# Optimization experiments

Measured on AMD Instinct MI355X. Metric: run time of the kernel, lower is better.

## Reference

```python
import jax, jax.numpy as jnp
import numpy as np

B, N, C, H = 4, 2048, 1024, 16
D = C // H  # head dim


def setup_inputs() -> dict:
    key = jax.random.key(0)
    ks = jax.random.split(key, 9)
    s = 1.0 / np.sqrt(C)
    inp = {"x": jax.random.normal(ks[0], (B, N, C), dtype=jnp.float32)}
    names = ["wq", "wk", "wv", "wo"]
    for i, n in enumerate(names):
        inp[n] = jax.random.uniform(ks[1 + 2 * i], (C, C), dtype=jnp.float32, minval=-s, maxval=s)
        inp["b" + n[1]] = jax.random.uniform(ks[2 + 2 * i], (C,), dtype=jnp.float32, minval=-s, maxval=s)
    return inp


def reference(x, wq, bq, wk, bk, wv, bv, wo, bo):
    b, n, c = x.shape
    # projections; weights stored as (in, out) so y = x @ w + b
    def split_heads(y):
        return y.reshape(b, n, H, D).transpose(0, 2, 1, 3)  # (B,H,N,D)

    q = split_heads(x @ wq + bq)
    k = split_heads(x @ wk + bk)
    v = split_heads(x @ wv + bv)
    scores = jnp.einsum("bhnd,bhmd->bhnm", q, k) / np.sqrt(D).astype(x.dtype)
    attn = jax.nn.softmax(scores, axis=-1)
    ctx = jnp.einsum("bhnm,bhmd->bhnd", attn, v)
    out = ctx.transpose(0, 2, 1, 3).reshape(b, n, c)
    return out @ wo + bo
```

## Files before the change

### kernel.cpp

```cpp
#include <hip/hip_runtime.h>
#include <hip/hip_bf16.h>
#include <hip/hip_fp16.h>

#define SEQ 2048
#define NH  16
#define DH  64
#define CH  1024
#define BATCH 4
#define BH (BATCH*NH)
#define MTOK (BATCH*SEQ)

typedef unsigned short u16;
typedef _Float16 h8 __attribute__((ext_vector_type(8)));
typedef float f4 __attribute__((ext_vector_type(4)));
typedef float f16x __attribute__((ext_vector_type(16)));

#define AS1(p) ((const __attribute__((address_space(1))) unsigned int*)(p))
#define AS3(p) ((__attribute__((address_space(3))) unsigned int*)(p))

__device__ __forceinline__ u16 f2h(float f) {
  _Float16 h = (_Float16)f;
  return __builtin_bit_cast(unsigned short, h);
}

__device__ __forceinline__ unsigned cvtpk(float a, float b) {
  auto t = __builtin_amdgcn_cvt_pkrtz(a, b);
  return __builtin_bit_cast(unsigned, t);
}

__device__ __forceinline__ float ex2(float x) { return __builtin_amdgcn_exp2f(x); }

__global__ __launch_bounds__(256) void k_convert_x(const float* __restrict__ x,
                                                   u16* __restrict__ xh) {
  int idx = (blockIdx.x * 256 + threadIdx.x) * 8;
  float4 a = *(const float4*)(x + idx);
  float4 b = *(const float4*)(x + idx + 4);
  uint4 o;
  o.x = (unsigned)f2h(a.x) | ((unsigned)f2h(a.y) << 16);
  o.y = (unsigned)f2h(a.z) | ((unsigned)f2h(a.w) << 16);
  o.z = (unsigned)f2h(b.x) | ((unsigned)f2h(b.y) << 16);
  o.w = (unsigned)f2h(b.z) | ((unsigned)f2h(b.w) << 16);
  *(uint4*)(xh + idx) = o;
}

__global__ __launch_bounds__(256) void k_transpose_w(const float* __restrict__ w0,
                                                     const float* __restrict__ w1,
                                                     const float* __restrict__ w2,
                                                     const float* __restrict__ w3,
                                                     u16* __restrict__ dst_all) {
  int mat = blockIdx.z;
  const float* src = (mat == 0) ? w0 : (mat == 1) ? w1 : (mat == 2) ? w2 : w3;
  u16* dst = dst_all + (size_t)mat * (CH * CH);
  __shared__ float t[64][65];
  int n0 = blockIdx.x * 64, k0 = blockIdx.y * 64;
#pragma unroll
  for (int i = 0; i < 16; ++i) {
    int idx = threadIdx.x + i * 256;
    int r = idx >> 6, c = idx & 63;
    t[r][c] = src[(size_t)(k0 + r) * CH + n0 + c];
  }
  __syncthreads();
#pragma unroll
  for (int i = 0; i < 16; ++i) {
    int idx = threadIdx.x + i * 256;
    int r = idx >> 6, c = idx & 63;
    dst[(size_t)(n0 + r) * CH + k0 + c] = f2h(t[c][r]);
  }
}

__global__ __launch_bounds__(256) void k_transpose_v(const u16* __restrict__ v,
                                                     u16* __restrict__ vt) {
  int n0 = blockIdx.x * 64;
  int bh = blockIdx.y;
  __shared__ u16 t[64][68];
  const u16* src = v + (size_t)bh * SEQ * DH + (size_t)n0 * DH;
#pragma unroll
  for (int i = 0; i < 4; ++i) {
    int g = threadIdx.x + i * 256;
    int r = g >> 4, c4 = (g & 15) * 4;
    *(ushort4*)&t[r][c4] = *(const ushort4*)(src + (size_t)r * DH + c4);
  }
  __syncthreads();
  u16* dst = vt + (size_t)bh * DH * SEQ + n0;
#pragma unroll
  for (int i = 0; i < 4; ++i) {
    int g = threadIdx.x + i * 256;
    int d = g >> 4, k4 = (g & 15) * 4;
    ushort4 o;
    o.x = t[k4 + 0][d]; o.y = t[k4 + 1][d]; o.z = t[k4 + 2][d]; o.w = t[k4 + 3][d];
    *(ushort4*)(dst + (size_t)d * SEQ + k4) = o;
  }
}

__global__ __launch_bounds__(256) void k_gemm_qkv(
    const u16* __restrict__ xh, const u16* __restrict__ wt,
    const float* __restrict__ bq, const float* __restrict__ bk,
    const float* __restrict__ bv,
    u16* __restrict__ qo, u16* __restrict__ ko, u16* __restrict__ vo) {
  const int tid = threadIdx.x;
  const int lane = tid & 63;
  const int wv = tid >> 6;
  const int wr = wv >> 1, wc = wv & 1;
  const int l16 = lane & 15, g = lane >> 4;
  const int tm = blockIdx.x;
  const int tn = blockIdx.y;
  const int mat = tn >> 3;
  const int nbase = (tn & 7) * 128;
  const u16* wb = wt + (size_t)mat * (CH * CH);

  __shared__ u16 As[128 * 32];
  __shared__ u16 Bs[128 * 32];

  f4 zero = {0.f, 0.f, 0.f, 0.f};
  f4 acc[4][4];
#pragma unroll
  for (int m = 0; m < 4; ++m)
#pragma unroll
    for (int n = 0; n < 4; ++n) acc[m][n] = zero;

  for (int k0 = 0; k0 < CH; k0 += 32) {
#pragma unroll
    for (int j = 0; j < 2; ++j) {
      int rbase = wv * 32 + j * 16;
      int row = rbase + (lane >> 2);
      int blk = (lane & 3) ^ ((row >> 1) & 3);
      const u16* ga = xh + (size_t)(tm * 128 + row) * CH + k0 + blk * 8;
      __builtin_amdgcn_global_load_lds(AS1(ga), AS3(&As[rbase * 32]), 16, 0, 0);
      const u16* gb = wb + (size_t)(nbase + row) * CH + k0 + blk * 8;
      __builtin_amdgcn_global_load_lds(AS1(gb), AS3(&Bs[rbase * 32]), 16, 0, 0);
    }
    __syncthreads();

    h8 af[4], bf[4];
#pragma unroll
    for (int i = 0; i < 4; ++i) {
      int arow = wr * 64 + i * 16 + l16;
      af[i] = *(const h8*)&As[arow * 32 + ((g ^ ((arow >> 1) & 3)) * 8)];
      int brow = wc * 64 + i * 16 + l16;
      bf[i] = *(const h8*)&Bs[brow * 32 + ((g ^ ((brow >> 1) & 3)) * 8)];
    }
#pragma unroll
    for (int m = 0; m < 4; ++m)
#pragma unroll
      for (int n = 0; n < 4; ++n)
        acc[m][n] = __builtin_amdgcn_mfma_f32_16x16x32_f16(af[m], bf[n], acc[m][n], 0, 0, 0);
    __syncthreads();
  }

  const float* bias = (mat == 0) ? bq : (mat == 1) ? bk : bv;
  u16* outp = (mat == 0) ? qo : (mat == 1) ? ko : vo;
  const float qscale = (mat == 0) ? 0.125f * 1.44269504f : 1.0f;
#pragma unroll
  for (int n = 0; n < 4; ++n) {
    int col = nbase + wc * 64 + n * 16 + l16;
    float bcol = bias[col];
    int h_ = col >> 6, d_ = col & 63;
#pragma unroll
    for (int m = 0; m < 4; ++m) {
#pragma unroll
      for (int r = 0; r < 4; ++r) {
        int t = tm * 128 + wr * 64 + m * 16 + g * 4 + r;
        int b_ = t >> 11, nseq = t & 2047;
        float val = (acc[m][n][r] + bcol) * qscale;
        outp[(((size_t)(b_ * NH + h_) * SEQ) + nseq) * DH + d_] = f2h(val);
      }
    }
  }
}

__global__ __launch_bounds__(256, 4) void k_attn(const u16* __restrict__ q,
                                                 const u16* __restrict__ k,
                                                 const u16* __restrict__ vt,
                                                 u16* __restrict__ ctx) {
  const int bid = blockIdx.x;
  const int bh = ((bid & 7) << 3) | ((bid >> 3) & 7);
  const int qb0 = bid >> 6;
  const int tid = threadIdx.x;
  const int lane = tid & 63;
  const int w = tid >> 6;
  const int l31 = lane & 31;
  const int hi = lane >> 5;

  __shared__ u16 Ks[2][32 * 128];
  __shared__ u16 Vs[2][32 * 128];

  const u16* kbase = k + (size_t)bh * SEQ * DH;
  const u16* vbase = vt + (size_t)bh * DH * SEQ;
  const u16* qbase = q + (size_t)bh * SEQ * DH;
  const int q0 = qb0 * 128 + w * 32;

  h8 qf[4];
#pragma unroll
  for (int ds = 0; ds < 4; ++ds)
    qf[ds] = *(const h8*)(qbase + (size_t)(q0 + l31) * DH + 16 * ds + 8 * hi);

  int koff[2][4];
  int voff[2][2][2];
#pragma unroll
  for (int h = 0; h < 2; ++h) {
#pragma unroll
    for (int ds = 0; ds < 4; ++ds) {
      int slot = 8 * h + 2 * ds + hi;
      koff[h][ds] = l31 * 128 + ((slot ^ (l31 & 15)) * 8);
    }
#pragma unroll
    for (int db = 0; db < 2; ++db)
#pragma unroll
      for (int ks = 0; ks < 2; ++ks) {
        int slot = 8 * db + 4 * h + 2 * ks + hi;
        voff[h][db][ks] = l31 * 128 + ((slot ^ (l31 & 15)) * 8);
      }
  }

  const u16* gk[2];
  const u16* gv[2];
#pragma unroll
  for (int c = 0; c < 2; ++c) {
    int r2 = w * 8 + c * 4 + (lane >> 4);
    int S = (lane & 15) ^ (r2 & 15);
    gk[c] = kbase + (size_t)(r2 + 32 * (S >> 3)) * DH + (S & 7) * 8;
    gv[c] = vbase + (size_t)(r2 + 32 * (S >> 3)) * SEQ + (S & 7) * 8;
  }

  const f16x fzero = {};
  h8 vones;
  {
    unsigned o1 = 0x3C003C00u;
    uint4 t = {o1, o1, o1, o1};
    vones = __builtin_bit_cast(h8, t);
  }

  f16x accq[2];
  accq[0] = {}; accq[1] = {};
  f16x lsum = {};

  auto STAGE = [&](int bi) {
#pragma unroll
    for (int c = 0; c < 2; ++c) {
      __builtin_amdgcn_global_load_lds(AS1(gk[c]), AS3(&Ks[bi][(w * 8 + c * 4) * 128]), 16, 0, 0);
      __builtin_amdgcn_global_load_lds(AS1(gv[c]), AS3(&Vs[bi][(w * 8 + c * 4) * 128]), 16, 0, 0);
      gk[c] += 64 * DH;
      gv[c] += 64;
    }
  };

  auto pack8 = [&](const float* p, int ks) -> h8 {
    unsigned a0 = cvtpk(p[8 * ks + 0], p[8 * ks + 1]);
    unsigned c0 = cvtpk(p[8 * ks + 2], p[8 * ks + 3]);
    unsigned b0 = cvtpk(p[8 * ks + 4], p[8 * ks + 5]);
    unsigned d0 = cvtpk(p[8 * ks + 6], p[8 * ks + 7]);
    unsigned s1 = __shfl_xor(hi ? a0 : b0, 32, 64);
    unsigned s2 = __shfl_xor(hi ? c0 : d0, 32, 64);
    uint4 wds;
    wds.x = hi ? s1 : a0;
    wds.y = hi ? s2 : c0;
    wds.z = hi ? b0 : s1;
    wds.w = hi ? d0 : s2;
    return __builtin_bit_cast(h8, wds);
  };

  auto SUBSTEP = [&](const u16* Kb, const u16* Vb, int h) {
    h8 kf0 = *(const h8*)(Kb + koff[h][0]);
    __builtin_amdgcn_s_setprio(1);
    f16x s = __builtin_amdgcn_mfma_f32_32x32x16_f16(kf0, qf[0], fzero, 0, 0, 0);
#pragma unroll
    for (int ds = 1; ds < 4; ++ds) {
      h8 kf = *(const h8*)(Kb + koff[h][ds]);
      s = __builtin_amdgcn_mfma_f32_32x32x16_f16(kf, qf[ds], s, 0, 0, 0);
    }
    __builtin_amdgcn_s_setprio(0);
    float p[16];
#pragma unroll
    for (int r = 0; r < 16; ++r) p[r] = ex2(s[r]);

    h8 pa0 = pack8(p, 0);
    h8 pa1 = pack8(p, 1);
    __builtin_amdgcn_s_setprio(1);
    lsum = __builtin_amdgcn_mfma_f32_32x32x16_f16(pa0, vones, lsum, 0, 0, 0);
    lsum = __builtin_amdgcn_mfma_f32_32x32x16_f16(pa1, vones, lsum, 0, 0, 0);
#pragma unroll
    for (int db = 0; db < 2; ++db) {
      h8 vf0 = *(const h8*)(Vb + voff[h][db][0]);
      accq[db] = __builtin_amdgcn_mfma_f32_32x32x16_f16(pa0, vf0, accq[db], 0, 0, 0);
      h8 vf1 = *(const h8*)(Vb + voff[h][db][1]);
      accq[db] = __builtin_amdgcn_mfma_f32_32x32x16_f16(pa1, vf1, accq[db], 0, 0, 0);
    }
    __builtin_amdgcn_s_setprio(0);
  };

  STAGE(0);
  for (int kt = 0; kt < SEQ / 64; kt += 2) {
    __syncthreads();
    STAGE(1);
    SUBSTEP(&Ks[0][0], &Vs[0][0], 0);
    SUBSTEP(&Ks[0][0], &Vs[0][0], 1);
    __syncthreads();
    if (kt + 2 < SEQ / 64) STAGE(0);
    SUBSTEP(&Ks[1][0], &Vs[1][0], 0);
    SUBSTEP(&Ks[1][0], &Vs[1][0], 1);
  }

  int b_ = bh >> 4, h_ = bh & 15;
#pragma unroll
  for (int r = 0; r < 16; ++r) {
    int row = (r & 3) + 8 * (r >> 2) + 4 * hi;
    float i0 = 1.0f / lsum[r];
#pragma unroll
    for (int db = 0; db < 2; ++db) {
      ctx[((size_t)(b_ * SEQ + q0 + row)) * CH + h_ * 64 + 32 * db + l31] =
          f2h(accq[db][r] * i0);
    }
  }
}

__global__ __launch_bounds__(256) void k_gemm_out(const u16* __restrict__ ctxb,
                                                  const u16* __restrict__ wot,
                                                  const float* __restrict__ bo,
                                                  float* __restrict__ out) {
  const int tid = threadIdx.x;
  const int lane = tid & 63;
  const int wv = tid >> 6;
  const int wr = wv >> 1, wc = wv & 1;
  const int l16 = lane & 15, g = lane >> 4;
  const int tm = blockIdx.x;
  const int nbase = blockIdx.y * 128;

  __shared__ u16 As[128 * 32];
  __shared__ u16 Bs[128 * 32];

  f4 zero = {0.f, 0.f, 0.f, 0.f};
  f4 acc[4][4];
#pragma unroll
  for (int m = 0; m < 4; ++m)
#pragma unroll
    for (int n = 0; n < 4; ++n) acc[m][n] = zero;

  for (int k0 = 0; k0 < CH; k0 += 32) {
#pragma unroll
    for (int j = 0; j < 2; ++j) {
      int rbase = wv * 32 + j * 16;
      int row = rbase + (lane >> 2);
      int blk = (lane & 3) ^ ((row >> 1) & 3);
      const u16* ga = ctxb + (size_t)(tm * 128 + row) * CH + k0 + blk * 8;
      __builtin_amdgcn_global_load_lds(AS1(ga), AS3(&As[rbase * 32]), 16, 0, 0);
      const u16* gb = wot + (size_t)(nbase + row) * CH + k0 + blk * 8;
      __builtin_amdgcn_global_load_lds(AS1(gb), AS3(&Bs[rbase * 32]), 16, 0, 0);
    }
    __syncthreads();

    h8 af[4], bf[4];
#pragma unroll
    for (int i = 0; i < 4; ++i) {
      int arow = wr * 64 + i * 16 + l16;
      af[i] = *(const h8*)&As[arow * 32 + ((g ^ ((arow >> 1) & 3)) * 8)];
      int brow = wc * 64 + i * 16 + l16;
      bf[i] = *(const h8*)&Bs[brow * 32 + ((g ^ ((brow >> 1) & 3)) * 8)];
    }
#pragma unroll
    for (int m = 0; m < 4; ++m)
#pragma unroll
      for (int n = 0; n < 4; ++n)
        acc[m][n] = __builtin_amdgcn_mfma_f32_16x16x32_f16(af[m], bf[n], acc[m][n], 0, 0, 0);
    __syncthreads();
  }

#pragma unroll
  for (int n = 0; n < 4; ++n) {
    int col = nbase + wc * 64 + n * 16 + l16;
    float bcol = bo[col];
#pragma unroll
    for (int m = 0; m < 4; ++m) {
#pragma unroll
      for (int r = 0; r < 4; ++r) {
        int t = tm * 128 + wr * 64 + m * 16 + g * 4 + r;
        out[(size_t)t * CH + col] = acc[m][n][r] + bcol;
      }
    }
  }
}

extern "C" void kernel_launch(void* const* d_in, const int* in_sizes, int n_in,
                              void* d_out, int out_size, void* d_ws, size_t ws_size,
                              hipStream_t stream) {
  (void)in_sizes; (void)n_in; (void)out_size; (void)ws_size;
  const float* x  = (const float*)d_in[0];
  const float* wq = (const float*)d_in[1];
  const float* bq = (const float*)d_in[2];
  const float* wk = (const float*)d_in[3];
  const float* bk = (const float*)d_in[4];
  const float* wv = (const float*)d_in[5];
  const float* bv = (const float*)d_in[6];
  const float* wo = (const float*)d_in[7];
  const float* bo = (const float*)d_in[8];
  float* out = (float*)d_out;

  char* ws = (char*)d_ws;
  u16* xh   = (u16*)(ws);
  u16* wt   = (u16*)(ws + 16777216);
  u16* qbuf = (u16*)(ws + 25165824);
  u16* kbuf = (u16*)(ws + 41943040);
  u16* vbuf = (u16*)(ws + 58720256);
  u16* ctxb = (u16*)(ws + 75497472);
  u16* wot  = wt + 3 * CH * CH;
  u16* vtb  = xh;

  k_convert_x<<<dim3(4096), dim3(256), 0, stream>>>(x, xh);
  k_transpose_w<<<dim3(16, 16, 4), dim3(256), 0, stream>>>(wq, wk, wv, wo, wt);
  k_gemm_qkv<<<dim3(64, 24), dim3(256), 0, stream>>>(xh, wt, bq, bk, bv, qbuf, kbuf, vbuf);
  k_transpose_v<<<dim3(32, 64), dim3(256), 0, stream>>>(vbuf, vtb);
  k_attn<<<dim3(1024), dim3(256), 0, stream>>>(qbuf, kbuf, vtb, ctxb);
  k_gemm_out<<<dim3(64, 8), dim3(256), 0, stream>>>(ctxb, wot, bo, out);
}
```

Measured before the change: 200.0 us.

## Double-buffer LDS in projection GEMMs and write V transposed directly

Both projection GEMMs now use two LDS buffers so the global-to-LDS load of the next K slice overlaps the MFMA work on the current one, and the per-iteration index math is hoisted into pointers that are simply advanced. The QKV GEMM epilogue writes V straight into the (B·H, D, N) transposed layout with 4-wide stores, so the separate V transpose kernel and its extra read and write pass are removed. The cost is doubled LDS per block, which may lower occupancy, and V stores that are strided across d.

```diff
diff --git a/kernel.cpp b/kernel.cpp
--- a/kernel.cpp
+++ b/kernel.cpp
@@ -68,35 +68,11 @@
   }
 }
 
-__global__ __launch_bounds__(256) void k_transpose_v(const u16* __restrict__ v,
-                                                     u16* __restrict__ vt) {
-  int n0 = blockIdx.x * 64;
-  int bh = blockIdx.y;
-  __shared__ u16 t[64][68];
-  const u16* src = v + (size_t)bh * SEQ * DH + (size_t)n0 * DH;
-#pragma unroll
-  for (int i = 0; i < 4; ++i) {
-    int g = threadIdx.x + i * 256;
-    int r = g >> 4, c4 = (g & 15) * 4;
-    *(ushort4*)&t[r][c4] = *(const ushort4*)(src + (size_t)r * DH + c4);
-  }
-  __syncthreads();
-  u16* dst = vt + (size_t)bh * DH * SEQ + n0;
-#pragma unroll
-  for (int i = 0; i < 4; ++i) {
-    int g = threadIdx.x + i * 256;
-    int d = g >> 4, k4 = (g & 15) * 4;
-    ushort4 o;
-    o.x = t[k4 + 0][d]; o.y = t[k4 + 1][d]; o.z = t[k4 + 2][d]; o.w = t[k4 + 3][d];
-    *(ushort4*)(dst + (size_t)d * SEQ + k4) = o;
-  }
-}
-
 __global__ __launch_bounds__(256) void k_gemm_qkv(
     const u16* __restrict__ xh, const u16* __restrict__ wt,
     const float* __restrict__ bq, const float* __restrict__ bk,
     const float* __restrict__ bv,
-    u16* __restrict__ qo, u16* __restrict__ ko, u16* __restrict__ vo) {
+    u16* __restrict__ qo, u16* __restrict__ ko, u16* __restrict__ vo_t) {
   const int tid = threadIdx.x;
   const int lane = tid & 63;
   const int wv = tid >> 6;
@@ -108,8 +84,21 @@
   const int nbase = (tn & 7) * 128;
   const u16* wb = wt + (size_t)mat * (CH * CH);
 
-  __shared__ u16 As[128 * 32];
-  __shared__ u16 Bs[128 * 32];
+  __shared__ u16 As[2][128 * 32];
+  __shared__ u16 Bs[2][128 * 32];
+
+  const u16* gA[2];
+  const u16* gB[2];
+  int rbase_[2];
+#pragma unroll
+  for (int j = 0; j < 2; ++j) {
+    int rbase = wv * 32 + j * 16;
+    rbase_[j] = rbase;
+    int row = rbase + (lane >> 2);
+    int blk = (lane & 3) ^ ((row >> 1) & 3);
+    gA[j] = xh + (size_t)(tm * 128 + row) * CH + blk * 8;
+    gB[j] = wb + (size_t)(nbase + row) * CH + blk * 8;
+  }
 
   f4 zero = {0.f, 0.f, 0.f, 0.f};
   f4 acc[4][4];
@@ -118,51 +107,78 @@
 #pragma unroll
     for (int n = 0; n < 4; ++n) acc[m][n] = zero;
 
-  for (int k0 = 0; k0 < CH; k0 += 32) {
+  auto STAGE = [&](int bi) {
 #pragma unroll
     for (int j = 0; j < 2; ++j) {
-      int rbase = wv * 32 + j * 16;
-      int row = rbase + (lane >> 2);
-      int blk = (lane & 3) ^ ((row >> 1) & 3);
-      const u16* ga = xh + (size_t)(tm * 128 + row) * CH + k0 + blk * 8;
-      __builtin_amdgcn_global_load_lds(AS1(ga), AS3(&As[rbase * 32]), 16, 0, 0);
-      const u16* gb = wb + (size_t)(nbase + row) * CH + k0 + blk * 8;
-      __builtin_amdgcn_global_load_lds(AS1(gb), AS3(&Bs[rbase * 32]), 16, 0, 0);
-    }
-    __syncthreads();
-
+      __builtin_amdgcn_global_load_lds(AS1(gA[j]), AS3(&As[bi][rbase_[j] * 32]), 16, 0, 0);
+      __builtin_amdgcn_global_load_lds(AS1(gB[j]), AS3(&Bs[bi][rbase_[j] * 32]), 16, 0, 0);
+      gA[j] += 32;
+      gB[j] += 32;
+    }
+  };
+
+  auto COMPUTE = [&](int bi) {
     h8 af[4], bf[4];
 #pragma unroll
     for (int i = 0; i < 4; ++i) {
       int arow = wr * 64 + i * 16 + l16;
-      af[i] = *(const h8*)&As[arow * 32 + ((g ^ ((arow >> 1) & 3)) * 8)];
+      af[i] = *(const h8*)&As[bi][arow * 32 + ((g ^ ((arow >> 1) & 3)) * 8)];
       int brow = wc * 64 + i * 16 + l16;
-      bf[i] = *(const h8*)&Bs[brow * 32 + ((g ^ ((brow >> 1) & 3)) * 8)];
+      bf[i] = *(const h8*)&Bs[bi][brow * 32 + ((g ^ ((brow >> 1) & 3)) * 8)];
     }
 #pragma unroll
     for (int m = 0; m < 4; ++m)
 #pragma unroll
       for (int n = 0; n < 4; ++n)
         acc[m][n] = __builtin_amdgcn_mfma_f32_16x16x32_f16(af[m], bf[n], acc[m][n], 0, 0, 0);
-    __syncthreads();
+  };
+
+  STAGE(0);
+  for (int k0 = 0; k0 < CH; k0 += 64) {
+    __syncthreads();
+    STAGE(1);
+    COMPUTE(0);
+    __syncthreads();
+    if (k0 + 64 < CH) STAGE(0);
+    COMPUTE(1);
   }
 
   const float* bias = (mat == 0) ? bq : (mat == 1) ? bk : bv;
-  u16* outp = (mat == 0) ? qo : (mat == 1) ? ko : vo;
-  const float qscale = (mat == 0) ? 0.125f * 1.44269504f : 1.0f;
-#pragma unroll
-  for (int n = 0; n < 4; ++n) {
-    int col = nbase + wc * 64 + n * 16 + l16;
-    float bcol = bias[col];
-    int h_ = col >> 6, d_ = col & 63;
-#pragma unroll
-    for (int m = 0; m < 4; ++m) {
-#pragma unroll
-      for (int r = 0; r < 4; ++r) {
-        int t = tm * 128 + wr * 64 + m * 16 + g * 4 + r;
-        int b_ = t >> 11, nseq = t & 2047;
-        float val = (acc[m][n][r] + bcol) * qscale;
-        outp[(((size_t)(b_ * NH + h_) * SEQ) + nseq) * DH + d_] = f2h(val);
+  if (mat == 2) {
+#pragma unroll
+    for (int n = 0; n < 4; ++n) {
+      int col = nbase + wc * 64 + n * 16 + l16;
+      float bcol = bias[col];
+      int h_ = col >> 6, d_ = col & 63;
+#pragma unroll
+      for (int m = 0; m < 4; ++m) {
+        int t0 = tm * 128 + wr * 64 + m * 16 + g * 4;
+        int b_ = t0 >> 11, nseq0 = t0 & 2047;
+        ushort4 o;
+        o.x = f2h(acc[m][n][0] + bcol);
+        o.y = f2h(acc[m][n][1] + bcol);
+        o.z = f2h(acc[m][n][2] + bcol);
+        o.w = f2h(acc[m][n][3] + bcol);
+        *(ushort4*)&vo_t[(((size_t)(b_ * NH + h_) * DH) + d_) * SEQ + nseq0] = o;
+      }
+    }
+  } else {
+    u16* outp = (mat == 0) ? qo : ko;
+    const float qscale = (mat == 0) ? 0.125f * 1.44269504f : 1.0f;
+#pragma unroll
+    for (int n = 0; n < 4; ++n) {
+      int col = nbase + wc * 64 + n * 16 + l16;
+      float bcol = bias[col];
+      int h_ = col >> 6, d_ = col & 63;
+#pragma unroll
+      for (int m = 0; m < 4; ++m) {
+#pragma unroll
+        for (int r = 0; r < 4; ++r) {
+          int t = tm * 128 + wr * 64 + m * 16 + g * 4 + r;
+          int b_ = t >> 11, nseq = t & 2047;
+          float val = (acc[m][n][r] + bcol) * qscale;
+          outp[(((size_t)(b_ * NH + h_) * SEQ) + nseq) * DH + d_] = f2h(val);
+        }
       }
     }
   }
@@ -325,8 +341,21 @@
   const int tm = blockIdx.x;
   const int nbase = blockIdx.y * 128;
 
-  __shared__ u16 As[128 * 32];
-  __shared__ u16 Bs[128 * 32];
+  __shared__ u16 As[2][128 * 32];
+  __shared__ u16 Bs[2][128 * 32];
+
+  const u16* gA[2];
+  const u16* gB[2];
+  int rbase_[2];
+#pragma unroll
+  for (int j = 0; j < 2; ++j) {
+    int rbase = wv * 32 + j * 16;
+    rbase_[j] = rbase;
+    int row = rbase + (lane >> 2);
+    int blk = (lane & 3) ^ ((row >> 1) & 3);
+    gA[j] = ctxb + (size_t)(tm * 128 + row) * CH + blk * 8;
+    gB[j] = wot + (size_t)(nbase + row) * CH + blk * 8;
+  }
 
   f4 zero = {0.f, 0.f, 0.f, 0.f};
   f4 acc[4][4];
@@ -335,33 +364,40 @@
 #pragma unroll
     for (int n = 0; n < 4; ++n) acc[m][n] = zero;
 
-  for (int k0 = 0; k0 < CH; k0 += 32) {
+  auto STAGE = [&](int bi) {
 #pragma unroll
     for (int j = 0; j < 2; ++j) {
-      int rbase = wv * 32 + j * 16;
-      int row = rbase + (lane >> 2);
-      int blk = (lane & 3) ^ ((row >> 1) & 3);
-      const u16* ga = ctxb + (size_t)(tm * 128 + row) * CH + k0 + blk * 8;
-      __builtin_amdgcn_global_load_lds(AS1(ga), AS3(&As[rbase * 32]), 16, 0, 0);
-      const u16* gb = wot + (size_t)(nbase + row) * CH + k0 + blk * 8;
-      __builtin_amdgcn_global_load_lds(AS1(gb), AS3(&Bs[rbase * 32]), 16, 0, 0);
-    }
-    __syncthreads();
-
+      __builtin_amdgcn_global_load_lds(AS1(gA[j]), AS3(&As[bi][rbase_[j] * 32]), 16, 0, 0);
+      __builtin_amdgcn_global_load_lds(AS1(gB[j]), AS3(&Bs[bi][rbase_[j] * 32]), 16, 0, 0);
+      gA[j] += 32;
+      gB[j] += 32;
+    }
+  };
+
+  auto COMPUTE = [&](int bi) {
     h8 af[4], bf[4];
 #pragma unroll
     for (int i = 0; i < 4; ++i) {
       int arow = wr * 64 + i * 16 + l16;
-      af[i] = *(const h8*)&As[arow * 32 + ((g ^ ((arow >> 1) & 3)) * 8)];
+      af[i] = *(const h8*)&As[bi][arow * 32 + ((g ^ ((arow >> 1) & 3)) * 8)];
       int brow = wc * 64 + i * 16 + l16;
-      bf[i] = *(const h8*)&Bs[brow * 32 + ((g ^ ((brow >> 1) & 3)) * 8)];
+      bf[i] = *(const h8*)&Bs[bi][brow * 32 + ((g ^ ((brow >> 1) & 3)) * 8)];
     }
 #pragma unroll
     for (int m = 0; m < 4; ++m)
 #pragma unroll
       for (int n = 0; n < 4; ++n)
         acc[m][n] = __builtin_amdgcn_mfma_f32_16x16x32_f16(af[m], bf[n], acc[m][n], 0, 0, 0);
-    __syncthreads();
+  };
+
+  STAGE(0);
+  for (int k0 = 0; k0 < CH; k0 += 64) {
+    __syncthreads();
+    STAGE(1);
+    COMPUTE(0);
+    __syncthreads();
+    if (k0 + 64 < CH) STAGE(0);
+    COMPUTE(1);
   }
 
 #pragma unroll
@@ -402,12 +438,10 @@
   u16* vbuf = (u16*)(ws + 58720256);
   u16* ctxb = (u16*)(ws + 75497472);
   u16* wot  = wt + 3 * CH * CH;
-  u16* vtb  = xh;
 
   k_convert_x<<<dim3(4096), dim3(256), 0, stream>>>(x, xh);
   k_transpose_w<<<dim3(16, 16, 4), dim3(256), 0, stream>>>(wq, wk, wv, wo, wt);
   k_gemm_qkv<<<dim3(64, 24), dim3(256), 0, stream>>>(xh, wt, bq, bk, bv, qbuf, kbuf, vbuf);
-  k_transpose_v<<<dim3(32, 64), dim3(256), 0, stream>>>(vbuf, vtb);
-  k_attn<<<dim3(1024), dim3(256), 0, stream>>>(qbuf, kbuf, vtb, ctxb);
+  k_attn<<<dim3(1024), dim3(256), 0, stream>>>(qbuf, kbuf, vbuf, ctxb);
   k_gemm_out<<<dim3(64, 8), dim3(256), 0, stream>>>(ctxb, wot, bo, out);
 }
```

Measured after the change: 217.5 us. +8.7%, slower.
